# Kernel tuning notes

Hardware: AMD Instinct MI355X
Metric: run time of the kernel (lower is better)

The kernel has to match this reference:

```python
import jax, jax.numpy as jnp
import numpy as np

N_NODES = 50000


def _add_self_loops(edge_index, n):
    loops = jnp.arange(n, dtype=edge_index.dtype)
    src = jnp.concatenate([edge_index[0], loops])
    dst = jnp.concatenate([edge_index[1], loops])
    return src, dst


def _gcn_norm(src, dst, n):
    # symmetric normalization deg^-1/2 (degrees include self-loops), as in PyG GCNConv
    ones = jnp.ones_like(dst, dtype=jnp.float32)
    deg = jax.ops.segment_sum(ones, dst, num_segments=n)
    dinv = jnp.where(deg > 0, jax.lax.rsqrt(deg), 0.0)
    return dinv[src] * dinv[dst]


def _gcn_conv(x, W, b, src, dst, norm, n):
    h = x @ W                                  # [N, d_out] dense transform first (d_out <= d_in)
    msg = h[src] * norm[:, None]               # gather + per-edge scale
    out = jax.ops.segment_sum(msg, dst, num_segments=n)  # scatter-add aggregation
    return out + b


def setup_inputs() -> dict:
    key = jax.random.key(0)
    ks = jax.random.split(key, 5)
    n, e = N_NODES, 1_600_000
    x = jax.random.normal(ks[0], (n, 512), dtype=jnp.float32)
    edge_index = jax.random.randint(ks[1], (2, e), 0, n, dtype=jnp.int64)
    def glorot(k, fi, fo):
        s = jnp.sqrt(6.0 / (fi + fo)).astype(jnp.float32)
        return jax.random.uniform(k, (fi, fo), jnp.float32, -s, s)
    return {
        "x": x,
        "edge_index": edge_index,
        "W0": glorot(ks[2], 512, 256), "b0": jnp.zeros((256,), jnp.float32),
        "W1": glorot(ks[3], 256, 256), "b1": jnp.zeros((256,), jnp.float32),
        "W2": glorot(ks[4], 256, 128), "b2": jnp.zeros((128,), jnp.float32),
    }


def reference(x, edge_index, W0, b0, W1, b1, W2, b2):
    n = x.shape[0]
    src, dst = _add_self_loops(edge_index, n)
    norm = _gcn_norm(src, dst, n)
    h = jax.nn.relu(_gcn_conv(x, W0, b0, src, dst, norm, n))
    h = jax.nn.relu(_gcn_conv(h, W1, b1, src, dst, norm, n))
    z = _gcn_conv(h, W2, b2, src, dst, norm, n)
    return z
```

## Files before the change

### kernel.cpp

```cpp
#include <hip/hip_runtime.h>
#include <hip/hip_bf16.h>
#include <type_traits>

#define NN 50000
#define CNT_S 16

typedef __attribute__((ext_vector_type(8))) short bf16x8;
typedef __attribute__((ext_vector_type(4))) float f32x4;
typedef unsigned int u32;

__device__ __forceinline__ ushort f2bf(float f) {
    unsigned u = __builtin_bit_cast(unsigned, f);
    unsigned r = (u + 0x7fffu + ((u >> 16) & 1u)) >> 16;
    return (ushort)r;
}
__device__ __forceinline__ float bflo(unsigned v) { return __builtin_bit_cast(float, v << 16); }
__device__ __forceinline__ float bfhi(unsigned v) { return __builtin_bit_cast(float, v & 0xffff0000u); }

__device__ __forceinline__ void gld16(const void* g, void* l) {
    __builtin_amdgcn_global_load_lds((const __attribute__((address_space(1))) u32*)g,
                                     (__attribute__((address_space(3))) u32*)l, 16, 0, 0);
}

__global__ void k_initw(int* cnt, int ncnt, const unsigned int* ei, int npairs, int* flag,
                        const float* __restrict__ W0, ushort* __restrict__ WT0,
                        const float* __restrict__ W1, ushort* __restrict__ WT1,
                        const float* __restrict__ W2, ushort* __restrict__ WT2) {
    int id = blockIdx.x * 256 + threadIdx.x;
    if (id < ncnt) cnt[id] = 0;
    if (blockIdx.x == 0) {
        __shared__ int any_nz;
        if (threadIdx.x == 0) any_nz = 0;
        __syncthreads();
        for (int p = threadIdx.x; p < npairs; p += blockDim.x) {
            if (ei[2 * p + 1] != 0u) atomicOr(&any_nz, 1);
        }
        __syncthreads();
        if (threadIdx.x == 0) *flag = (any_nz == 0) ? 1 : 0;
    }
    const float* W; ushort* WT; int K, N, loc;
    if (id < 131072)      { W = W0; WT = WT0; K = 512; N = 256; loc = id; }
    else if (id < 196608) { W = W1; WT = WT1; K = 256; N = 256; loc = id - 131072; }
    else if (id < 229376) { W = W2; WT = WT2; K = 256; N = 128; loc = id - 196608; }
    else return;
    int nn = loc / K, k = loc - nn * K;
    WT[loc] = f2bf(W[(long long)k * N + nn]);
}

__device__ __forceinline__ int load_idx(const void* ei, long long pos, int is64) {
    return is64 ? (int)(((const long long*)ei)[pos]) : ((const int*)ei)[pos];
}

__global__ void k_count(const void* ei, long long E, const int* flag,
                        int* cnt, int* __restrict__ ord) {
    long long e = (long long)blockIdx.x * blockDim.x + threadIdx.x;
    if (e < E) {
        int dst = load_idx(ei, E + e, *flag);
        ord[e] = atomicAdd(&cnt[(long long)dst * CNT_S], 1);
    }
}

__global__ __launch_bounds__(1024) void k_scan_a(const int* __restrict__ cnt,
                                                 int* __restrict__ bsum,
                                                 float* __restrict__ dinv, int n) {
    __shared__ int wsum[16];
    int i = blockIdx.x * 1024 + threadIdx.x;
    int lane = (int)threadIdx.x & 63, w = (int)threadIdx.x >> 6;
    int v = (i < n) ? cnt[(long long)i * CNT_S] : 0;
    int pv = (v + 7) & ~7;
    if (i < n) dinv[i] = rsqrtf((float)(v + 1));
    int s = pv;
#pragma unroll
    for (int off = 1; off < 64; off <<= 1) s += __shfl_xor(s, off);
    if (lane == 0) wsum[w] = s;
    __syncthreads();
    if (threadIdx.x == 0) {
        int t = 0;
#pragma unroll
        for (int k = 0; k < 16; ++k) t += wsum[k];
        bsum[blockIdx.x] = t;
    }
}

__global__ void k_scan_b(const int* __restrict__ bsum, int* __restrict__ bbase,
                         int* __restrict__ offs_n, int nb) {
    int lane = (int)threadIdx.x;
    int v = (lane < nb) ? bsum[lane] : 0;
    int x = v;
#pragma unroll
    for (int off = 1; off < 64; off <<= 1) {
        int y = __shfl_up(x, off);
        if (lane >= off) x += y;
    }
    if (lane < nb) bbase[lane] = x - v;
    if (lane == nb - 1) *offs_n = x;
}

__global__ __launch_bounds__(1024) void k_scan_c(const int* __restrict__ cnt,
                                                 const int* __restrict__ bbase,
                                                 int* __restrict__ offs, int n) {
    __shared__ int wsum[16];
    int i = blockIdx.x * 1024 + threadIdx.x;
    int lane = (int)threadIdx.x & 63, w = (int)threadIdx.x >> 6;
    int v = (i < n) ? cnt[(long long)i * CNT_S] : 0;
    int pv = (v + 7) & ~7;
    int x = pv;
#pragma unroll
    for (int off = 1; off < 64; off <<= 1) {
        int y = __shfl_up(x, off);
        if (lane >= off) x += y;
    }
    if (lane == 63) wsum[w] = x;
    __syncthreads();
    if (w == 0) {
        int pvv = (lane < 16) ? wsum[lane] : 0;
#pragma unroll
        for (int off = 1; off < 16; off <<= 1) {
            int py = __shfl_up(pvv, off);
            if (lane >= off) pvv += py;
        }
        if (lane < 16) wsum[lane] = pvv;
    }
    __syncthreads();
    int wbase = (w > 0) ? wsum[w - 1] : 0;
    if (i < n) offs[i] = bbase[blockIdx.x] + wbase + x - pv;
}

#define KE 8
__global__ void k_bucket(const void* ei, long long E, const int* __restrict__ flag,
                         const float* __restrict__ dinv, const int* __restrict__ offs,
                         const int* __restrict__ ord, int2* __restrict__ epk,
                         const int* __restrict__ cnt, int n, int nchunk_e, int pn) {
    int p = blockIdx.x & 7;
    int c = blockIdx.x >> 3;
    int lo = p * pn;
    int hi = lo + pn; if (hi > n) hi = n;
    if (c < nchunk_e) {
        int is64 = *flag;
        long long base = (long long)c * (256 * KE) + threadIdx.x;
#pragma unroll
        for (int k = 0; k < KE; ++k) {
            long long e = base + k * 256;
            if (e < E) {
                int dst = load_idx(ei, E + e, is64);
                if (dst >= lo && dst < hi) {
                    int src = load_idx(ei, e, is64);
                    int pos = offs[dst] + ord[e];
                    epk[pos] = make_int2(src, __builtin_bit_cast(int, dinv[src] * dinv[dst]));
                }
            }
        }
    } else {
        int i = lo + (c - nchunk_e) * 256 + (int)threadIdx.x;
        if (i < hi) {
            int b = offs[i] + cnt[(long long)i * CNT_S], en = offs[i + 1];
            for (int j = b; j < en; ++j) epk[j] = make_int2(0, 0);
        }
    }
}

__global__ void k_x2bf(const float* __restrict__ x, ushort* __restrict__ xbf, long long n8) {
    long long id = (long long)blockIdx.x * blockDim.x + threadIdx.x;
    if (id < n8) {
        const float* src = x + id * 8;
        float4 f0 = *(const float4*)src;
        float4 f1 = *(const float4*)(src + 4);
        ushort tmp[8] = {f2bf(f0.x), f2bf(f0.y), f2bf(f0.z), f2bf(f0.w),
                         f2bf(f1.x), f2bf(f1.y), f2bf(f1.z), f2bf(f1.w)};
        *(uint4*)&xbf[id * 8] = *(uint4*)tmp;
    }
}

#define LOFF(r, s) (((r) * 8 + ((s) ^ ((r) & 7))) * 8)

template <typename TA>
__global__ __launch_bounds__(256) void k_gemm_mfma(const TA* __restrict__ A,
                                                   const ushort* __restrict__ WT,
                                                   ushort* __restrict__ C,
                                                   int M, int N, int K) {
    __shared__ ushort As[8192];
    __shared__ ushort Bs[8192];
    int t = threadIdx.x;
    int lane = t & 63;
    int w = t >> 6;
    int wr = (w >> 1) * 64, wc = (w & 1) * 64;
    int m0 = blockIdx.y * 128, n0 = blockIdx.x * 128;

    f32x4 acc[4][4] = {};

    for (int k0 = 0; k0 < K; k0 += 64) {
#pragma unroll
        for (int j = 0; j < 4; ++j) {
            int id = (w * 4 + j) * 64 + lane;
            int r = id >> 3, sp = id & 7;
            int s = sp ^ (r & 7);
            gld16(WT + (long long)(n0 + r) * K + k0 + s * 8, &Bs[(r * 8 + sp) * 8]);
        }
        if constexpr (std::is_same<TA, float>::value) {
#pragma unroll
            for (int j = 0; j < 4; ++j) {
                int id = t + j * 256;
                int r = id >> 3, s = id & 7;
                int grow = m0 + r;
                if (grow < M) {
                    const float* src = A + (long long)grow * K + k0 + s * 8;
                    float4 f0 = *(const float4*)src;
                    float4 f1 = *(const float4*)(src + 4);
                    ushort tmp[8] = {f2bf(f0.x), f2bf(f0.y), f2bf(f0.z), f2bf(f0.w),
                                     f2bf(f1.x), f2bf(f1.y), f2bf(f1.z), f2bf(f1.w)};
                    *(uint4*)&As[LOFF(r, s)] = *(uint4*)tmp;
                }
            }
        } else {
#pragma unroll
            for (int j = 0; j < 4; ++j) {
                int rbase = (w * 4 + j) * 8;
                if (m0 + rbase < M) {
                    int id = rbase * 8 + lane;
                    int r = id >> 3, sp = id & 7;
                    int s = sp ^ (r & 7);
                    gld16((const ushort*)A + (long long)(m0 + r) * K + k0 + s * 8,
                          &As[(r * 8 + sp) * 8]);
                }
            }
        }
        __syncthreads();
#pragma unroll
        for (int kk = 0; kk < 2; ++kk) {
            int ks = kk * 4 + (lane >> 4);
            bf16x8 a[4], b[4];
#pragma unroll
            for (int m = 0; m < 4; ++m)
                a[m] = *(bf16x8*)&As[LOFF(wr + m * 16 + (lane & 15), ks)];
#pragma unroll
            for (int nn = 0; nn < 4; ++nn)
                b[nn] = *(bf16x8*)&Bs[LOFF(wc + nn * 16 + (lane & 15), ks)];
#pragma unroll
            for (int m = 0; m < 4; ++m)
#pragma unroll
                for (int nn = 0; nn < 4; ++nn)
                    acc[m][nn] = __builtin_amdgcn_mfma_f32_16x16x32_bf16(a[m], b[nn], acc[m][nn], 0, 0, 0);
        }
        __syncthreads();
    }
#pragma unroll
    for (int m = 0; m < 4; ++m) {
#pragma unroll
        for (int i = 0; i < 4; ++i) {
            int row = m0 + wr + m * 16 + (lane >> 4) * 4 + i;
            if (row < M) {
#pragma unroll
                for (int nn = 0; nn < 4; ++nn) {
                    int col = n0 + wc + nn * 16 + (lane & 15);
                    C[(long long)row * N + col] = f2bf(acc[m][nn][i]);
                }
            }
        }
    }
}

template <int DT, bool RELU, bool OUTF32>
__global__ __launch_bounds__(128) void k_aggs(const ushort* __restrict__ h,
                                              const int* __restrict__ offs,
                                              const int2* __restrict__ epk,
                                              const float* __restrict__ dinv,
                                              const float* __restrict__ bias,
                                              void* __restrict__ outp, int n, int foff) {
    int node = __builtin_amdgcn_readfirstlane((int)(blockIdx.x * 2 + (threadIdx.x >> 6)));
    if (node >= n) return;
    int t = (int)threadIdx.x & 63;
    float di = dinv[node];
    float dii = di * di;

    unsigned v0 = *(const unsigned*)&h[(long long)node * DT + foff + t * 2];
    float2 bs = *(const float2*)&bias[foff + t * 2];
    float a0 = bs.x + dii * bflo(v0);
    float a1 = bs.y + dii * bfhi(v0);

    int s = offs[node], e = offs[node + 1];

    for (int j = s; j < e; j += 8) {
        int2 p[8];
#pragma unroll
        for (int u = 0; u < 8; ++u) p[u] = epk[j + u];
        unsigned v[8];
#pragma unroll
        for (int u = 0; u < 8; ++u)
            v[u] = *(const unsigned*)&h[(long long)p[u].x * DT + foff + t * 2];
#pragma unroll
        for (int u = 0; u < 8; ++u) {
            float wgt = __builtin_bit_cast(float, p[u].y);
            a0 += wgt * bflo(v[u]);
            a1 += wgt * bfhi(v[u]);
        }
    }

    if (RELU) { a0 = fmaxf(a0, 0.f); a1 = fmaxf(a1, 0.f); }
    long long oidx = ((long long)node * DT + foff) / 2 + t;
    if constexpr (OUTF32) {
        ((float2*)outp)[oidx] = make_float2(a0, a1);
    } else {
        unsigned pk = (unsigned)f2bf(a0) | ((unsigned)f2bf(a1) << 16);
        ((unsigned*)outp)[oidx] = pk;
    }
}

extern "C" void kernel_launch(void* const* d_in, const int* in_sizes, int n_in,
                              void* d_out, int out_size, void* d_ws, size_t ws_size,
                              hipStream_t stream) {
    const float* x  = (const float*)d_in[0];
    const void*  ei = d_in[1];
    const float* W0 = (const float*)d_in[2];
    const float* b0 = (const float*)d_in[3];
    const float* W1 = (const float*)d_in[4];
    const float* b1 = (const float*)d_in[5];
    const float* W2 = (const float*)d_in[6];
    const float* b2 = (const float*)d_in[7];
    float* out = (float*)d_out;

    const int n = NN;
    const long long E = (long long)in_sizes[1] / 2;
    const int ncnt = n * CNT_S;
    const int nbscan = (n + 1023) / 1024;

    char* ws = (char*)d_ws;
    int*    cnt  = (int*)(ws);
    int*    offs = (int*)(ws + 3400 * 1024);
    float*  dinv = (float*)(ws + 3700 * 1024);
    int*    flag = (int*)(ws + 3960 * 1024);
    int*    bsum = (int*)(ws + 3964 * 1024);
    int*    bbase= (int*)(ws + 3968 * 1024);
    int2*   epk  = (int2*)(ws + 4ll * 1024 * 1024);
    ushort* WT0  = (ushort*)(ws + 20ll * 1024 * 1024);
    ushort* WT1  = (ushort*)(ws + 20ll * 1024 * 1024 + 512 * 1024);
    ushort* WT2  = (ushort*)(ws + 20ll * 1024 * 1024 + 768 * 1024);
    ushort* hA   = (ushort*)(ws + 21ll * 1024 * 1024);
    ushort* hB   = (ushort*)(ws + 47ll * 1024 * 1024);
    ushort* xbf  = (ushort*)(ws + 73ll * 1024 * 1024);
    int*    ord  = (int*)hA;
    const size_t need_xbf = 73ll * 1024 * 1024 + 51200000ll;
    const bool have_xbf = (ws_size >= need_xbf);

    {
        int nb = (ncnt + 255) / 256;
        k_initw<<<nb, 256, 0, stream>>>(cnt, ncnt, (const unsigned int*)ei, 4096, flag,
                                        W0, WT0, W1, WT1, W2, WT2);
    }

    k_count<<<(int)((E + 255) / 256), 256, 0, stream>>>(ei, E, flag, cnt, ord);
    k_scan_a<<<nbscan, 1024, 0, stream>>>(cnt, bsum, dinv, n);
    k_scan_b<<<1, 64, 0, stream>>>(bsum, bbase, &offs[n], nbscan);
    k_scan_c<<<nbscan, 1024, 0, stream>>>(cnt, bbase, offs, n);
    {
        int nchunk_e = (int)((E + 256 * KE - 1) / (256 * KE));
        int pn = (n + 7) / 8;
        int nchunk_pad = (pn + 255) / 256;
        k_bucket<<<8 * (nchunk_e + nchunk_pad), 256, 0, stream>>>(
            ei, E, flag, dinv, offs, ord, epk, cnt, n, nchunk_e, pn);
    }
    if (have_xbf) {
        long long n8 = (long long)n * 512 / 8;
        k_x2bf<<<(int)((n8 + 255) / 256), 256, 0, stream>>>(x, xbf, n8);
    }

    int mt = (n + 127) / 128;
    int nb2 = (n + 1) / 2;

    if (have_xbf) {
        k_gemm_mfma<ushort><<<dim3(2, mt), 256, 0, stream>>>(xbf, WT0, hA, n, 256, 512);
    } else {
        k_gemm_mfma<float><<<dim3(2, mt), 256, 0, stream>>>(x, WT0, hA, n, 256, 512);
    }
    k_aggs<256, true, false><<<nb2, 128, 0, stream>>>(hA, offs, epk, dinv, b0, hB, n, 0);
    k_aggs<256, true, false><<<nb2, 128, 0, stream>>>(hA, offs, epk, dinv, b0, hB, n, 128);

    k_gemm_mfma<ushort><<<dim3(2, mt), 256, 0, stream>>>(hB, WT1, hA, n, 256, 256);
    k_aggs<256, true, false><<<nb2, 128, 0, stream>>>(hA, offs, epk, dinv, b1, hB, n, 0);
    k_aggs<256, true, false><<<nb2, 128, 0, stream>>>(hA, offs, epk, dinv, b1, hB, n, 128);

    k_gemm_mfma<ushort><<<dim3(1, mt), 256, 0, stream>>>(hB, WT2, hA, n, 128, 256);
    k_aggs<128, false, true><<<nb2, 128, 0, stream>>>(hA, offs, epk, dinv, b2, out, n, 0);
}
```

Measured before the change: 450.8 us.

## Replace global atomic edge counting with per-chunk LDS histograms and column prefix scan

Replaces the global-atomic degree count, which wrote a per-edge ordinal array, with per-(partition, chunk) shared-memory histograms. A column scan over chunks then yields per-chunk bases, degrees and dinv. The scatter kernel recomputes each edge's slot with LDS atomics plus those per-chunk bases, so the ord array and the padded global counter array are gone. This removes contended global atomics and the large counter init, at the cost of a serial column scan over about 98 chunks per node and a second pass over edge indices.

```diff
diff --git a/kernel.cpp b/kernel.cpp
--- a/kernel.cpp
+++ b/kernel.cpp
@@ -3,7 +3,9 @@
 #include <type_traits>
 
 #define NN 50000
-#define CNT_S 16
+#define NP 8
+#define PN ((NN + NP - 1) / NP)
+#define KE2 64
 
 typedef __attribute__((ext_vector_type(8))) short bf16x8;
 typedef __attribute__((ext_vector_type(4))) float f32x4;
@@ -22,12 +24,11 @@
                                      (__attribute__((address_space(3))) u32*)l, 16, 0, 0);
 }
 
-__global__ void k_initw(int* cnt, int ncnt, const unsigned int* ei, int npairs, int* flag,
+__global__ void k_initw(const unsigned int* ei, int npairs, int* flag,
                         const float* __restrict__ W0, ushort* __restrict__ WT0,
                         const float* __restrict__ W1, ushort* __restrict__ WT1,
                         const float* __restrict__ W2, ushort* __restrict__ WT2) {
     int id = blockIdx.x * 256 + threadIdx.x;
-    if (id < ncnt) cnt[id] = 0;
     if (blockIdx.x == 0) {
         __shared__ int any_nz;
         if (threadIdx.x == 0) any_nz = 0;
@@ -51,24 +52,53 @@
     return is64 ? (int)(((const long long*)ei)[pos]) : ((const int*)ei)[pos];
 }
 
-__global__ void k_count(const void* ei, long long E, const int* flag,
-                        int* cnt, int* __restrict__ ord) {
-    long long e = (long long)blockIdx.x * blockDim.x + threadIdx.x;
-    if (e < E) {
-        int dst = load_idx(ei, E + e, *flag);
-        ord[e] = atomicAdd(&cnt[(long long)dst * CNT_S], 1);
-    }
+__global__ __launch_bounds__(256) void k_hist(const void* ei, long long E,
+                                              const int* __restrict__ flag,
+                                              int* __restrict__ hist, int n, int C) {
+    __shared__ int lh[PN];
+    int p = blockIdx.x & (NP - 1), c = blockIdx.x >> 3;
+    int lo = p * PN;
+    int hi = lo + PN; if (hi > n) hi = n;
+    int len = hi - lo;
+    for (int i = threadIdx.x; i < len; i += 256) lh[i] = 0;
+    __syncthreads();
+    int is64 = *flag;
+    long long cbase = (long long)c * (256 * KE2);
+    for (int k = 0; k < KE2; ++k) {
+        long long e = cbase + k * 256 + threadIdx.x;
+        if (e < E) {
+            int dst = load_idx(ei, E + e, is64);
+            if (dst >= lo && dst < hi) atomicAdd(&lh[dst - lo], 1);
+        }
+    }
+    __syncthreads();
+    int* gh = hist + ((long long)p * C + c) * PN;
+    for (int i = threadIdx.x; i < len; i += 256) gh[i] = lh[i];
+}
+
+__global__ void k_cscan(int* __restrict__ hist, int* __restrict__ cnt,
+                        float* __restrict__ dinv, int n, int C) {
+    int i = blockIdx.x * 256 + threadIdx.x;
+    if (i >= n) return;
+    int p = i / PN, li = i - p * PN;
+    int* col = hist + ((long long)p * C) * PN + li;
+    int acc = 0;
+    for (int c = 0; c < C; ++c) {
+        int t = col[(long long)c * PN];
+        col[(long long)c * PN] = acc;
+        acc += t;
+    }
+    cnt[i] = acc;
+    dinv[i] = rsqrtf((float)(acc + 1));
 }
 
 __global__ __launch_bounds__(1024) void k_scan_a(const int* __restrict__ cnt,
-                                                 int* __restrict__ bsum,
-                                                 float* __restrict__ dinv, int n) {
+                                                 int* __restrict__ bsum, int n) {
     __shared__ int wsum[16];
     int i = blockIdx.x * 1024 + threadIdx.x;
     int lane = (int)threadIdx.x & 63, w = (int)threadIdx.x >> 6;
-    int v = (i < n) ? cnt[(long long)i * CNT_S] : 0;
+    int v = (i < n) ? cnt[i] : 0;
     int pv = (v + 7) & ~7;
-    if (i < n) dinv[i] = rsqrtf((float)(v + 1));
     int s = pv;
 #pragma unroll
     for (int off = 1; off < 64; off <<= 1) s += __shfl_xor(s, off);
@@ -102,7 +132,7 @@
     __shared__ int wsum[16];
     int i = blockIdx.x * 1024 + threadIdx.x;
     int lane = (int)threadIdx.x & 63, w = (int)threadIdx.x >> 6;
-    int v = (i < n) ? cnt[(long long)i * CNT_S] : 0;
+    int v = (i < n) ? cnt[i] : 0;
     int pv = (v + 7) & ~7;
     int x = pv;
 #pragma unroll
@@ -126,34 +156,38 @@
     if (i < n) offs[i] = bbase[blockIdx.x] + wbase + x - pv;
 }
 
-#define KE 8
-__global__ void k_bucket(const void* ei, long long E, const int* __restrict__ flag,
-                         const float* __restrict__ dinv, const int* __restrict__ offs,
-                         const int* __restrict__ ord, int2* __restrict__ epk,
-                         const int* __restrict__ cnt, int n, int nchunk_e, int pn) {
-    int p = blockIdx.x & 7;
-    int c = blockIdx.x >> 3;
-    int lo = p * pn;
-    int hi = lo + pn; if (hi > n) hi = n;
-    if (c < nchunk_e) {
+__global__ __launch_bounds__(256) void k_scat(const void* ei, long long E,
+                        const int* __restrict__ flag,
+                        const float* __restrict__ dinv, const int* __restrict__ offs,
+                        const int* __restrict__ hist, int2* __restrict__ epk,
+                        const int* __restrict__ cnt, int n, int C) {
+    int p = blockIdx.x & (NP - 1), c = blockIdx.x >> 3;
+    int lo = p * PN;
+    int hi = lo + PN; if (hi > n) hi = n;
+    if (c < C) {
+        __shared__ int cur[PN];
+        int len = hi - lo;
+        for (int i = threadIdx.x; i < len; i += 256) cur[i] = 0;
+        __syncthreads();
         int is64 = *flag;
-        long long base = (long long)c * (256 * KE) + threadIdx.x;
-#pragma unroll
-        for (int k = 0; k < KE; ++k) {
-            long long e = base + k * 256;
+        const int* cb = hist + ((long long)p * C + c) * PN;
+        long long cbase = (long long)c * (256 * KE2);
+        for (int k = 0; k < KE2; ++k) {
+            long long e = cbase + k * 256 + threadIdx.x;
             if (e < E) {
                 int dst = load_idx(ei, E + e, is64);
                 if (dst >= lo && dst < hi) {
+                    int loc = atomicAdd(&cur[dst - lo], 1);
                     int src = load_idx(ei, e, is64);
-                    int pos = offs[dst] + ord[e];
+                    int pos = offs[dst] + cb[dst - lo] + loc;
                     epk[pos] = make_int2(src, __builtin_bit_cast(int, dinv[src] * dinv[dst]));
                 }
             }
         }
     } else {
-        int i = lo + (c - nchunk_e) * 256 + (int)threadIdx.x;
+        int i = lo + (c - C) * 256 + (int)threadIdx.x;
         if (i < hi) {
-            int b = offs[i] + cnt[(long long)i * CNT_S], en = offs[i + 1];
+            int b = offs[i] + cnt[i], en = offs[i + 1];
             for (int j = b; j < en; ++j) epk[j] = make_int2(0, 0);
         }
     }
@@ -320,8 +354,8 @@
 
     const int n = NN;
     const long long E = (long long)in_sizes[1] / 2;
-    const int ncnt = n * CNT_S;
     const int nbscan = (n + 1023) / 1024;
+    const int C = (int)((E + 256 * KE2 - 1) / (256 * KE2));
 
     char* ws = (char*)d_ws;
     int*    cnt  = (int*)(ws);
@@ -337,26 +371,21 @@
     ushort* hA   = (ushort*)(ws + 21ll * 1024 * 1024);
     ushort* hB   = (ushort*)(ws + 47ll * 1024 * 1024);
     ushort* xbf  = (ushort*)(ws + 73ll * 1024 * 1024);
-    int*    ord  = (int*)hA;
+    int*    hist = (int*)hB;
     const size_t need_xbf = 73ll * 1024 * 1024 + 51200000ll;
     const bool have_xbf = (ws_size >= need_xbf);
 
-    {
-        int nb = (ncnt + 255) / 256;
-        k_initw<<<nb, 256, 0, stream>>>(cnt, ncnt, (const unsigned int*)ei, 4096, flag,
-                                        W0, WT0, W1, WT1, W2, WT2);
-    }
-
-    k_count<<<(int)((E + 255) / 256), 256, 0, stream>>>(ei, E, flag, cnt, ord);
-    k_scan_a<<<nbscan, 1024, 0, stream>>>(cnt, bsum, dinv, n);
+    k_initw<<<(229376 + 255) / 256, 256, 0, stream>>>((const unsigned int*)ei, 4096, flag,
+                                                      W0, WT0, W1, WT1, W2, WT2);
+
+    k_hist<<<NP * C, 256, 0, stream>>>(ei, E, flag, hist, n, C);
+    k_cscan<<<(n + 255) / 256, 256, 0, stream>>>(hist, cnt, dinv, n, C);
+    k_scan_a<<<nbscan, 1024, 0, stream>>>(cnt, bsum, n);
     k_scan_b<<<1, 64, 0, stream>>>(bsum, bbase, &offs[n], nbscan);
     k_scan_c<<<nbscan, 1024, 0, stream>>>(cnt, bbase, offs, n);
     {
-        int nchunk_e = (int)((E + 256 * KE - 1) / (256 * KE));
-        int pn = (n + 7) / 8;
-        int nchunk_pad = (pn + 255) / 256;
-        k_bucket<<<8 * (nchunk_e + nchunk_pad), 256, 0, stream>>>(
-            ei, E, flag, dinv, offs, ord, epk, cnt, n, nchunk_e, pn);
+        int npad = (PN + 255) / 256;
+        k_scat<<<NP * (C + npad), 256, 0, stream>>>(ei, E, flag, dinv, offs, hist, epk, cnt, n, C);
     }
     if (have_xbf) {
         long long n8 = (long long)n * 512 / 8;
```

After: 469.4 us. 4.1% more time.

## Fuse x-to-bf16 conversion into init and first GEMM into count kernel

Applied to the files above, without the earlier changes.

The fp32-to-bf16 conversion of x moves into extra blocks of the init kernel, and the first-layer GEMM runs as extra blocks of the degree-count kernel. Independent preprocessing and compute then share launches and can overlap, which cuts two kernel launches and lets the atomic counting hide behind the GEMM. The ord scratch buffer moves from hA to hB so it does not collide with the GEMM output. The fused count/GEMM kernel reserves 32KB of shared memory for every block, including the count blocks, which may lower their occupancy.

```diff
diff --git a/kernel.cpp b/kernel.cpp
--- a/kernel.cpp
+++ b/kernel.cpp
@@ -22,10 +22,28 @@
                                      (__attribute__((address_space(3))) u32*)l, 16, 0, 0);
 }
 
+__device__ __forceinline__ int load_idx(const void* ei, long long pos, int is64) {
+    return is64 ? (int)(((const long long*)ei)[pos]) : ((const int*)ei)[pos];
+}
+
 __global__ void k_initw(int* cnt, int ncnt, const unsigned int* ei, int npairs, int* flag,
                         const float* __restrict__ W0, ushort* __restrict__ WT0,
                         const float* __restrict__ W1, ushort* __restrict__ WT1,
-                        const float* __restrict__ W2, ushort* __restrict__ WT2) {
+                        const float* __restrict__ W2, ushort* __restrict__ WT2,
+                        const float* __restrict__ x, ushort* __restrict__ xbf,
+                        long long n8, int nbi) {
+    if ((int)blockIdx.x >= nbi) {
+        long long id = (long long)(blockIdx.x - nbi) * 256 + threadIdx.x;
+        if (id < n8) {
+            const float* src = x + id * 8;
+            float4 f0 = *(const float4*)src;
+            float4 f1 = *(const float4*)(src + 4);
+            ushort tmp[8] = {f2bf(f0.x), f2bf(f0.y), f2bf(f0.z), f2bf(f0.w),
+                             f2bf(f1.x), f2bf(f1.y), f2bf(f1.z), f2bf(f1.w)};
+            *(uint4*)&xbf[id * 8] = *(uint4*)tmp;
+        }
+        return;
+    }
     int id = blockIdx.x * 256 + threadIdx.x;
     if (id < ncnt) cnt[id] = 0;
     if (blockIdx.x == 0) {
@@ -47,8 +65,89 @@
     WT[loc] = f2bf(W[(long long)k * N + nn]);
 }
 
-__device__ __forceinline__ int load_idx(const void* ei, long long pos, int is64) {
-    return is64 ? (int)(((const long long*)ei)[pos]) : ((const int*)ei)[pos];
+#define LOFF(r, s) (((r) * 8 + ((s) ^ ((r) & 7))) * 8)
+
+__device__ __forceinline__ void gemm_tile_u16(const ushort* __restrict__ A,
+                                              const ushort* __restrict__ WT,
+                                              ushort* __restrict__ C,
+                                              int M, int N, int K, int m0, int n0,
+                                              ushort* As, ushort* Bs) {
+    int t = threadIdx.x;
+    int lane = t & 63;
+    int w = t >> 6;
+    int wr = (w >> 1) * 64, wc = (w & 1) * 64;
+    f32x4 acc[4][4] = {};
+    for (int k0 = 0; k0 < K; k0 += 64) {
+#pragma unroll
+        for (int j = 0; j < 4; ++j) {
+            int id = (w * 4 + j) * 64 + lane;
+            int r = id >> 3, sp = id & 7;
+            int s = sp ^ (r & 7);
+            gld16(WT + (long long)(n0 + r) * K + k0 + s * 8, &Bs[(r * 8 + sp) * 8]);
+        }
+#pragma unroll
+        for (int j = 0; j < 4; ++j) {
+            int rbase = (w * 4 + j) * 8;
+            if (m0 + rbase < M) {
+                int id = rbase * 8 + lane;
+                int r = id >> 3, sp = id & 7;
+                int s = sp ^ (r & 7);
+                gld16(A + (long long)(m0 + r) * K + k0 + s * 8, &As[(r * 8 + sp) * 8]);
+            }
+        }
+        __syncthreads();
+#pragma unroll
+        for (int kk = 0; kk < 2; ++kk) {
+            int ks = kk * 4 + (lane >> 4);
+            bf16x8 a[4], b[4];
+#pragma unroll
+            for (int m = 0; m < 4; ++m)
+                a[m] = *(bf16x8*)&As[LOFF(wr + m * 16 + (lane & 15), ks)];
+#pragma unroll
+            for (int nn = 0; nn < 4; ++nn)
+                b[nn] = *(bf16x8*)&Bs[LOFF(wc + nn * 16 + (lane & 15), ks)];
+#pragma unroll
+            for (int m = 0; m < 4; ++m)
+#pragma unroll
+                for (int nn = 0; nn < 4; ++nn)
+                    acc[m][nn] = __builtin_amdgcn_mfma_f32_16x16x32_bf16(a[m], b[nn], acc[m][nn], 0, 0, 0);
+        }
+        __syncthreads();
+    }
+#pragma unroll
+    for (int m = 0; m < 4; ++m) {
+#pragma unroll
+        for (int i = 0; i < 4; ++i) {
+            int row = m0 + wr + m * 16 + (lane >> 4) * 4 + i;
+            if (row < M) {
+#pragma unroll
+                for (int nn = 0; nn < 4; ++nn) {
+                    int col = n0 + wc + nn * 16 + (lane & 15);
+                    C[(long long)row * N + col] = f2bf(acc[m][nn][i]);
+                }
+            }
+        }
+    }
+}
+
+__global__ __launch_bounds__(256) void k_countg(const void* ei, long long E,
+                                                const int* __restrict__ flag,
+                                                int* cnt, int* __restrict__ ord, int nbc,
+                                                const ushort* __restrict__ A,
+                                                const ushort* __restrict__ WT,
+                                                ushort* __restrict__ C, int M, int N, int K) {
+    __shared__ ushort As[8192];
+    __shared__ ushort Bs[8192];
+    if ((int)blockIdx.x < nbc) {
+        long long e = (long long)blockIdx.x * 256 + threadIdx.x;
+        if (e < E) {
+            int dst = load_idx(ei, E + e, *flag);
+            ord[e] = atomicAdd(&cnt[(long long)dst * CNT_S], 1);
+        }
+        return;
+    }
+    int b = (int)blockIdx.x - nbc;
+    gemm_tile_u16(A, WT, C, M, N, K, (b >> 1) * 128, (b & 1) * 128, As, Bs);
 }
 
 __global__ void k_count(const void* ei, long long E, const int* flag,
@@ -159,20 +258,6 @@
     }
 }
 
-__global__ void k_x2bf(const float* __restrict__ x, ushort* __restrict__ xbf, long long n8) {
-    long long id = (long long)blockIdx.x * blockDim.x + threadIdx.x;
-    if (id < n8) {
-        const float* src = x + id * 8;
-        float4 f0 = *(const float4*)src;
-        float4 f1 = *(const float4*)(src + 4);
-        ushort tmp[8] = {f2bf(f0.x), f2bf(f0.y), f2bf(f0.z), f2bf(f0.w),
-                         f2bf(f1.x), f2bf(f1.y), f2bf(f1.z), f2bf(f1.w)};
-        *(uint4*)&xbf[id * 8] = *(uint4*)tmp;
-    }
-}
-
-#define LOFF(r, s) (((r) * 8 + ((s) ^ ((r) & 7))) * 8)
-
 template <typename TA>
 __global__ __launch_bounds__(256) void k_gemm_mfma(const TA* __restrict__ A,
                                                    const ushort* __restrict__ WT,
@@ -180,23 +265,21 @@
                                                    int M, int N, int K) {
     __shared__ ushort As[8192];
     __shared__ ushort Bs[8192];
-    int t = threadIdx.x;
-    int lane = t & 63;
-    int w = t >> 6;
-    int wr = (w >> 1) * 64, wc = (w & 1) * 64;
     int m0 = blockIdx.y * 128, n0 = blockIdx.x * 128;
-
-    f32x4 acc[4][4] = {};
-
-    for (int k0 = 0; k0 < K; k0 += 64) {
-#pragma unroll
-        for (int j = 0; j < 4; ++j) {
-            int id = (w * 4 + j) * 64 + lane;
-            int r = id >> 3, sp = id & 7;
-            int s = sp ^ (r & 7);
-            gld16(WT + (long long)(n0 + r) * K + k0 + s * 8, &Bs[(r * 8 + sp) * 8]);
-        }
-        if constexpr (std::is_same<TA, float>::value) {
+    if constexpr (std::is_same<TA, float>::value) {
+        int t = threadIdx.x;
+        int lane = t & 63;
+        int w = t >> 6;
+        int wr = (w >> 1) * 64, wc = (w & 1) * 64;
+        f32x4 acc[4][4] = {};
+        for (int k0 = 0; k0 < K; k0 += 64) {
+#pragma unroll
+            for (int j = 0; j < 4; ++j) {
+                int id = (w * 4 + j) * 64 + lane;
+                int r = id >> 3, sp = id & 7;
+                int s = sp ^ (r & 7);
+                gld16(WT + (long long)(n0 + r) * K + k0 + s * 8, &Bs[(r * 8 + sp) * 8]);
+            }
 #pragma unroll
             for (int j = 0; j < 4; ++j) {
                 int id = t + j * 256;
@@ -211,51 +294,41 @@
                     *(uint4*)&As[LOFF(r, s)] = *(uint4*)tmp;
                 }
             }
-        } else {
-#pragma unroll
-            for (int j = 0; j < 4; ++j) {
-                int rbase = (w * 4 + j) * 8;
-                if (m0 + rbase < M) {
-                    int id = rbase * 8 + lane;
-                    int r = id >> 3, sp = id & 7;
-                    int s = sp ^ (r & 7);
-                    gld16((const ushort*)A + (long long)(m0 + r) * K + k0 + s * 8,
-                          &As[(r * 8 + sp) * 8]);
+            __syncthreads();
+#pragma unroll
+            for (int kk = 0; kk < 2; ++kk) {
+                int ks = kk * 4 + (lane >> 4);
+                bf16x8 a[4], b[4];
+#pragma unroll
+                for (int m = 0; m < 4; ++m)
+                    a[m] = *(bf16x8*)&As[LOFF(wr + m * 16 + (lane & 15), ks)];
+#pragma unroll
+                for (int nn = 0; nn < 4; ++nn)
+                    b[nn] = *(bf16x8*)&Bs[LOFF(wc + nn * 16 + (lane & 15), ks)];
+#pragma unroll
+                for (int m = 0; m < 4; ++m)
+#pragma unroll
+                    for (int nn = 0; nn < 4; ++nn)
+                        acc[m][nn] = __builtin_amdgcn_mfma_f32_16x16x32_bf16(a[m], b[nn], acc[m][nn], 0, 0, 0);
+            }
+            __syncthreads();
+        }
+#pragma unroll
+        for (int m = 0; m < 4; ++m) {
+#pragma unroll
+            for (int i = 0; i < 4; ++i) {
+                int row = m0 + wr + m * 16 + (lane >> 4) * 4 + i;
+                if (row < M) {
+#pragma unroll
+                    for (int nn = 0; nn < 4; ++nn) {
+                        int col = n0 + wc + nn * 16 + (lane & 15);
+                        C[(long long)row * N + col] = f2bf(acc[m][nn][i]);
+                    }
                 }
             }
         }
-        __syncthreads();
-#pragma unroll
-        for (int kk = 0; kk < 2; ++kk) {
-            int ks = kk * 4 + (lane >> 4);
-            bf16x8 a[4], b[4];
-#pragma unroll
-            for (int m = 0; m < 4; ++m)
-                a[m] = *(bf16x8*)&As[LOFF(wr + m * 16 + (lane & 15), ks)];
-#pragma unroll
-            for (int nn = 0; nn < 4; ++nn)
-                b[nn] = *(bf16x8*)&Bs[LOFF(wc + nn * 16 + (lane & 15), ks)];
-#pragma unroll
-            for (int m = 0; m < 4; ++m)
-#pragma unroll
-                for (int nn = 0; nn < 4; ++nn)
-                    acc[m][nn] = __builtin_amdgcn_mfma_f32_16x16x32_bf16(a[m], b[nn], acc[m][nn], 0, 0, 0);
-        }
-        __syncthreads();
-    }
-#pragma unroll
-    for (int m = 0; m < 4; ++m) {
-#pragma unroll
-        for (int i = 0; i < 4; ++i) {
-            int row = m0 + wr + m * 16 + (lane >> 4) * 4 + i;
-            if (row < M) {
-#pragma unroll
-                for (int nn = 0; nn < 4; ++nn) {
-                    int col = n0 + wc + nn * 16 + (lane & 15);
-                    C[(long long)row * N + col] = f2bf(acc[m][nn][i]);
-                }
-            }
-        }
+    } else {
+        gemm_tile_u16(A, WT, C, M, N, K, m0, n0, As, Bs);
     }
 }
 
@@ -337,17 +410,28 @@
     ushort* hA   = (ushort*)(ws + 21ll * 1024 * 1024);
     ushort* hB   = (ushort*)(ws + 47ll * 1024 * 1024);
     ushort* xbf  = (ushort*)(ws + 73ll * 1024 * 1024);
-    int*    ord  = (int*)hA;
+    int*    ord  = (int*)hB;
     const size_t need_xbf = 73ll * 1024 * 1024 + 51200000ll;
     const bool have_xbf = (ws_size >= need_xbf);
 
-    {
-        int nb = (ncnt + 255) / 256;
-        k_initw<<<nb, 256, 0, stream>>>(cnt, ncnt, (const unsigned int*)ei, 4096, flag,
-                                        W0, WT0, W1, WT1, W2, WT2);
-    }
-
-    k_count<<<(int)((E + 255) / 256), 256, 0, stream>>>(ei, E, flag, cnt, ord);
+    const int nbi = (ncnt + 255) / 256;
+    const long long n8 = (long long)n * 512 / 8;
+    const int nbx = have_xbf ? (int)((n8 + 255) / 256) : 0;
+
+    k_initw<<<nbi + nbx, 256, 0, stream>>>(cnt, ncnt, (const unsigned int*)ei, 4096, flag,
+                                           W0, WT0, W1, WT1, W2, WT2, x, xbf, n8, nbi);
+
+    int mt = (n + 127) / 128;
+    int nb2 = (n + 1) / 2;
+    const int nbc = (int)((E + 255) / 256);
+
+    if (have_xbf) {
+        k_countg<<<nbc + 2 * mt, 256, 0, stream>>>(ei, E, flag, cnt, ord, nbc,
+                                                   xbf, WT0, hA, n, 256, 512);
+    } else {
+        k_count<<<nbc, 256, 0, stream>>>(ei, E, flag, cnt, ord);
+        k_gemm_mfma<float><<<dim3(2, mt), 256, 0, stream>>>(x, WT0, hA, n, 256, 512);
+    }
     k_scan_a<<<nbscan, 1024, 0, stream>>>(cnt, bsum, dinv, n);
     k_scan_b<<<1, 64, 0, stream>>>(bsum, bbase, &offs[n], nbscan);
     k_scan_c<<<nbscan, 1024, 0, stream>>>(cnt, bbase, offs, n);
@@ -358,19 +442,7 @@
         k_bucket<<<8 * (nchunk_e + nchunk_pad), 256, 0, stream>>>(
             ei, E, flag, dinv, offs, ord, epk, cnt, n, nchunk_e, pn);
     }
-    if (have_xbf) {
-        long long n8 = (long long)n * 512 / 8;
-        k_x2bf<<<(int)((n8 + 255) / 256), 256, 0, stream>>>(x, xbf, n8);
-    }
-
-    int mt = (n + 127) / 128;
-    int nb2 = (n + 1) / 2;
-
-    if (have_xbf) {
-        k_gemm_mfma<ushort><<<dim3(2, mt), 256, 0, stream>>>(xbf, WT0, hA, n, 256, 512);
-    } else {
-        k_gemm_mfma<float><<<dim3(2, mt), 256, 0, stream>>>(x, WT0, hA, n, 256, 512);
-    }
+
     k_aggs<256, true, false><<<nb2, 128, 0, stream>>>(hA, offs, epk, dinv, b0, hB, n, 0);
     k_aggs<256, true, false><<<nb2, 128, 0, stream>>>(hA, offs, epk, dinv, b0, hB, n, 128);
 
```

After: 437.9 us. -2.8%, faster.
